# Kernel optimization log

Hardware: AMD Instinct MI355X
Metric: run time of the kernel (lower is better)

Reference implementation:

```python
import jax, jax.numpy as jnp
import numpy as np

N = 50000
E = 1600000
IN_DIM = 256
HID = 64
OUT = 16
NEG_SLOPE = 0.01


def setup_inputs() -> dict:
    key = jax.random.key(0)
    ks = jax.random.split(key, 6)
    local_features = jax.random.normal(ks[0], (N, IN_DIM), dtype=jnp.float32)
    edge_index = jax.random.randint(ks[1], (2, E), 0, N, dtype=jnp.int32)
    W0 = jax.random.normal(ks[2], (IN_DIM, HID), dtype=jnp.float32) * 0.05
    a0 = jax.random.normal(ks[3], (2 * HID, 1), dtype=jnp.float32) * 0.05
    W1 = jax.random.normal(ks[4], (HID, OUT), dtype=jnp.float32) * 0.05
    a1 = jax.random.normal(ks[5], (2 * OUT, 1), dtype=jnp.float32) * 0.05
    return {"local_features": local_features, "edge_index": edge_index,
            "W0": W0, "a0": a0, "W1": W1, "a1": a1}


def _segment_softmax(scores, seg, num_segments):
    # softmax over edges sharing the same row (destination) id
    smax = jax.ops.segment_max(scores, seg, num_segments=num_segments)
    ex = jnp.exp(scores - smax[seg])
    ssum = jax.ops.segment_sum(ex, seg, num_segments=num_segments)
    return ex / ssum[seg]


def _gat_layer(H, row, col, W, a, apply_elu):
    d = W.shape[1]
    Hw = H @ W                                   # [N, d]
    # score_e = leaky_relu([Hw[row] || Hw[col]] @ a) = leaky_relu(pr[row] + pc[col])
    pr = Hw @ a[:d, 0]                           # [N]
    pc = Hw @ a[d:, 0]                           # [N]
    s = pr[row] + pc[col]                        # [E]
    s = jnp.where(s >= 0, s, NEG_SLOPE * s)      # leaky_relu
    att = _segment_softmax(s, row, Hw.shape[0])  # per-row sparse softmax (dim=1)
    # out[row] = sum_e att_e * Hw[col_e]
    out = jax.ops.segment_sum(att[:, None] * Hw[col], row, num_segments=Hw.shape[0])
    if apply_elu:
        out = jnp.where(out > 0, out, jnp.expm1(out))  # elu
    return out


def reference(local_features, edge_index, W0, a0, W1, a1):
    row = edge_index[0]
    col = edge_index[1]
    H = _gat_layer(local_features, row, col, W0, a0, apply_elu=True)
    H = _gat_layer(H, row, col, W1, a1, apply_elu=False)
    return jax.nn.log_softmax(H, axis=1)
```

## Files before the change

### kernel.cpp

```cpp
#include <hip/hip_runtime.h>
#include <hip/hip_bf16.h>
#include <math.h>

#define NN 50000
#define NE 1600000
#define BSH 9
#define BCK 98
#define BCAP 20480

typedef __attribute__((ext_vector_type(8))) short bf16x8;
typedef __attribute__((ext_vector_type(4))) float f32x4;

__device__ __forceinline__ short f2bf(float f) {
    return (short)((__float_as_uint(f) + 0x8000u) >> 16);
}
__device__ __forceinline__ float bf2f(ushort u) {
    return __uint_as_float(((unsigned)u) << 16);
}
__device__ __forceinline__ unsigned enc_f(float f) {
    unsigned u = __float_as_uint(f);
    return (u & 0x80000000u) ? ~u : (u | 0x80000000u);
}
__device__ __forceinline__ float dec_f(unsigned e) {
    return (e & 0x80000000u) ? __uint_as_float(e & 0x7FFFFFFFu)
                             : __uint_as_float(~e);
}

__global__ void initcur_kernel(int* __restrict__ gcursor) {
    int b = threadIdx.x;
    if (b < BCK) gcursor[b] = b * BCAP;
}

__global__ void __launch_bounds__(1024) binA_kernel(
        const int* __restrict__ row, const int* __restrict__ col,
        int* __restrict__ gcursor, unsigned* __restrict__ staging) {
    __shared__ unsigned lds_stage[8192];
    __shared__ unsigned lds_addr[8192];
    __shared__ int lds_cnt[128];
    __shared__ int lds_off[128];
    __shared__ int wg_goff[128];
    __shared__ int wtot[2];
    int t = threadIdx.x;
    int lane = t & 63;
    int w = t >> 6;

    for (int cb = blockIdx.x * 8192; cb < NE; cb += gridDim.x * 8192) {
        int cnt_edges = NE - cb; if (cnt_edges > 8192) cnt_edges = 8192;
        if (t < 128) lds_cnt[t] = 0;
        __syncthreads();
        int myb[8]; int mylo[8]; unsigned mypk[8];
        #pragma unroll
        for (int i = 0; i < 8; ++i) {
            int idx = i * 1024 + t;
            myb[i] = -1;
            if (idx < cnt_edges) {
                int e = cb + idx;
                int r = row[e], c = col[e];
                int b = r >> BSH;
                myb[i] = b;
                mypk[i] = ((unsigned)(r & 511) << 16) | (unsigned)c;
                mylo[i] = atomicAdd(&lds_cnt[b], 1);
            }
        }
        __syncthreads();
        int v = (t < 128) ? lds_cnt[t] : 0;
        int x = v;
        #pragma unroll
        for (int off = 1; off < 64; off <<= 1) {
            int y = __shfl_up(x, off);
            if (lane >= off) x += y;
        }
        if (t < 128 && lane == 63) wtot[w] = x;
        __syncthreads();
        int add = (w == 1) ? wtot[0] : 0;
        if (t < 128) lds_off[t] = x - v + add;
        if (t < BCK) {
            int cc = lds_cnt[t];
            wg_goff[t] = cc ? atomicAdd(&gcursor[t], cc) : 0;
        }
        __syncthreads();
        #pragma unroll
        for (int i = 0; i < 8; ++i) if (myb[i] >= 0) {
            int p = lds_off[myb[i]] + mylo[i];
            lds_stage[p] = mypk[i];
            lds_addr[p] = (unsigned)(wg_goff[myb[i]] + mylo[i]);
        }
        __syncthreads();
        for (int i = t; i < cnt_edges; i += 1024)
            staging[lds_addr[i]] = lds_stage[i];
        __syncthreads();
    }
}

__global__ void bucketscan_kernel(const int* __restrict__ gcursor,
                                  int* __restrict__ bbase,
                                  int* __restrict__ rowptr) {
    __shared__ int wt0;
    int t = threadIdx.x;
    int lane = t & 63;
    int w = t >> 6;
    int v = (t < BCK) ? (gcursor[t] - t * BCAP) : 0;
    int x = v;
    #pragma unroll
    for (int off = 1; off < 64; off <<= 1) {
        int y = __shfl_up(x, off);
        if (lane >= off) x += y;
    }
    if (w == 0 && lane == 63) wt0 = x;
    __syncthreads();
    int excl = x - v + ((w == 1) ? wt0 : 0);
    if (t < BCK) bbase[t] = excl;
    if (t == BCK - 1) { bbase[BCK] = excl + v; rowptr[NN] = excl + v; }
}

__global__ void __launch_bounds__(1024) binB_kernel(
        const int* __restrict__ bbase,
        const unsigned* __restrict__ staging,
        int* __restrict__ rowptr,
        ushort* __restrict__ colperm) {
    __shared__ int cur[512];
    __shared__ int lexcl[512];
    __shared__ int wls[8];
    __shared__ ushort lds_col[BCAP];
    int b = blockIdx.x;
    int t = threadIdx.x;
    int lane = t & 63;
    int w = t >> 6;
    int rbase = b << BSH;
    int nrows = NN - rbase; if (nrows > 512) nrows = 512;
    int gbase = bbase[b];
    int cnt = bbase[b + 1] - gbase;
    if (cnt > BCAP) cnt = BCAP;
    const unsigned* sb = staging + (size_t)b * BCAP;

    if (t < 512) cur[t] = 0;
    __syncthreads();
    for (int i = t; i < cnt; i += 1024)
        atomicAdd(&cur[sb[i] >> 16], 1);
    __syncthreads();
    int v = 0, x = 0;
    if (t < 512) {
        v = cur[t];
        x = v;
        #pragma unroll
        for (int off = 1; off < 64; off <<= 1) {
            int y = __shfl_up(x, off);
            if (lane >= off) x += y;
        }
        if (lane == 63) wls[w] = x;
    }
    __syncthreads();
    if (t < 8) {
        int s = wls[t];
        #pragma unroll
        for (int off = 1; off < 8; off <<= 1) {
            int y = __shfl_up(s, off, 8);
            if ((t & 7) >= off) s += y;
        }
        wls[t] = s;
    }
    __syncthreads();
    if (t < 512) {
        int e = x - v + ((w > 0) ? wls[w - 1] : 0);
        lexcl[t] = e;
        if (t < nrows) rowptr[rbase + t] = gbase + e;
    }
    __syncthreads();
    if (t < 512) cur[t] = lexcl[t];
    __syncthreads();
    for (int i = t; i < cnt; i += 1024) {
        unsigned e = sb[i];
        int pos = atomicAdd(&cur[e >> 16], 1);
        lds_col[pos] = (ushort)(e & 0xFFFFu);
    }
    __syncthreads();
    for (int i = t; i < cnt; i += 1024)
        colperm[gbase + i] = lds_col[i];
}

__global__ void pcmax_kernel(const float* __restrict__ pc, unsigned* __restrict__ out) {
    int i = blockIdx.x * 256 + threadIdx.x;
    float v = (i < NN) ? pc[i] : -1e30f;
    #pragma unroll
    for (int off = 32; off; off >>= 1) v = fmaxf(v, __shfl_xor(v, off));
    if ((threadIdx.x & 63) == 0) atomicMax(out, enc_f(v));
}

__global__ void __launch_bounds__(256) gemm0_kernel(
        const float* __restrict__ X,
        const float* __restrict__ W,
        const float* __restrict__ a,
        __hip_bfloat16* __restrict__ Hwb,
        float* __restrict__ pr,
        float* __restrict__ pc) {
    __shared__ ushort Wt[64 * 264];
    int tid = threadIdx.x;
    int lane = tid & 63;
    int wid = tid >> 6;
    int c = lane & 15;
    int quad = lane >> 4;

    for (int i = tid; i < 256 * 64; i += 256) {
        int k = i >> 6, n = i & 63;
        Wt[n * 264 + k] = (ushort)f2bf(W[i]);
    }
    __syncthreads();

    int row0 = blockIdx.x * 64 + wid * 16;
    int arow = row0 + c; if (arow >= NN) arow = NN - 1;
    const float* xbase = X + (size_t)arow * 256 + quad * 8;
    const ushort* wt0 = &Wt[(0 * 16 + c) * 264 + quad * 8];
    const ushort* wt1 = &Wt[(1 * 16 + c) * 264 + quad * 8];
    const ushort* wt2 = &Wt[(2 * 16 + c) * 264 + quad * 8];
    const ushort* wt3 = &Wt[(3 * 16 + c) * 264 + quad * 8];

    f32x4 acc0 = {0.f,0.f,0.f,0.f}, acc1 = {0.f,0.f,0.f,0.f};
    f32x4 acc2 = {0.f,0.f,0.f,0.f}, acc3 = {0.f,0.f,0.f,0.f};

#pragma unroll
    for (int k0 = 0; k0 < 256; k0 += 32) {
        float4 xa = *(const float4*)(xbase + k0);
        float4 xb = *(const float4*)(xbase + k0 + 4);
        bf16x8 af;
        af[0] = f2bf(xa.x); af[1] = f2bf(xa.y); af[2] = f2bf(xa.z); af[3] = f2bf(xa.w);
        af[4] = f2bf(xb.x); af[5] = f2bf(xb.y); af[6] = f2bf(xb.z); af[7] = f2bf(xb.w);
        bf16x8 b0 = *(const bf16x8*)(wt0 + k0);
        bf16x8 b1 = *(const bf16x8*)(wt1 + k0);
        bf16x8 b2 = *(const bf16x8*)(wt2 + k0);
        bf16x8 b3 = *(const bf16x8*)(wt3 + k0);
        acc0 = __builtin_amdgcn_mfma_f32_16x16x32_bf16(af, b0, acc0, 0, 0, 0);
        acc1 = __builtin_amdgcn_mfma_f32_16x16x32_bf16(af, b1, acc1, 0, 0, 0);
        acc2 = __builtin_amdgcn_mfma_f32_16x16x32_bf16(af, b2, acc2, 0, 0, 0);
        acc3 = __builtin_amdgcn_mfma_f32_16x16x32_bf16(af, b3, acc3, 0, 0, 0);
    }

    float aA0 = a[c],      aA1 = a[16 + c],      aA2 = a[32 + c],      aA3 = a[48 + c];
    float aB0 = a[64 + c], aB1 = a[80 + c],      aB2 = a[96 + c],      aB3 = a[112 + c];

#pragma unroll
    for (int r = 0; r < 4; ++r) {
        int row = row0 + quad * 4 + r;
        float v0 = acc0[r], v1 = acc1[r], v2 = acc2[r], v3 = acc3[r];
        if (row < NN) {
            __hip_bfloat16* hp = Hwb + (size_t)row * 64 + c;
            hp[0]  = __float2bfloat16(v0);
            hp[16] = __float2bfloat16(v1);
            hp[32] = __float2bfloat16(v2);
            hp[48] = __float2bfloat16(v3);
        }
        float pv = v0 * aA0 + v1 * aA1 + v2 * aA2 + v3 * aA3;
        float qv = v0 * aB0 + v1 * aB1 + v2 * aB2 + v3 * aB3;
#pragma unroll
        for (int off = 8; off; off >>= 1) {
            pv += __shfl_xor(pv, off);
            qv += __shfl_xor(qv, off);
        }
        if (c == 0 && row < NN) { pr[row] = pv; pc[row] = qv; }
    }
}

__global__ void __launch_bounds__(256) node0_kernel(
        const int* __restrict__ rowptr,
        const ushort* __restrict__ colperm,
        const float* __restrict__ pr,
        const float* __restrict__ pc,
        const unsigned* __restrict__ pcmax,
        const ushort* __restrict__ Hwb,
        float* __restrict__ H1) {
    int lane = threadIdx.x & 63;
    int node = blockIdx.x * 4 + (threadIdx.x >> 6);
    if (node >= NN) return;
    int k = lane & 15, q = lane >> 4;
    int start = rowptr[node], end = rowptr[node + 1];
    float pri = pr[node];
    float m = pri + dec_f(*pcmax);
    m = (m >= 0.f) ? m : 0.01f * m;

    float wsum = 0.f;
    float acc0 = 0.f, acc1 = 0.f, acc2 = 0.f, acc3 = 0.f;
    for (int base = start; base < end; base += 64) {
        int n = end - base; if (n > 64) n = 64;
        float wv = 0.f; int cv = 0;
        if (lane < n) {
            cv = (int)colperm[base + lane];
            float s = pri + pc[cv];
            s = (s >= 0.f) ? s : 0.01f * s;
            wv = expf(s - m);
        }
        wsum += wv;
        int iters = (n + 3) >> 2;
        #pragma unroll 4
        for (int jj = 0; jj < iters; ++jj) {
            int j = jj * 4 + q;
            int jc = (j < n) ? j : 0;
            float wj = __shfl(wv, jc);
            if (j >= n) wj = 0.f;
            int cj = __shfl(cv, jc);
            ushort4 hv = *(const ushort4*)(Hwb + (size_t)cj * 64 + k * 4);
            acc0 = fmaf(wj, bf2f(hv.x), acc0);
            acc1 = fmaf(wj, bf2f(hv.y), acc1);
            acc2 = fmaf(wj, bf2f(hv.z), acc2);
            acc3 = fmaf(wj, bf2f(hv.w), acc3);
        }
    }
#pragma unroll
    for (int off = 32; off; off >>= 1) wsum += __shfl_xor(wsum, off);
    acc0 += __shfl_xor(acc0, 16); acc0 += __shfl_xor(acc0, 32);
    acc1 += __shfl_xor(acc1, 16); acc1 += __shfl_xor(acc1, 32);
    acc2 += __shfl_xor(acc2, 16); acc2 += __shfl_xor(acc2, 32);
    acc3 += __shfl_xor(acc3, 16); acc3 += __shfl_xor(acc3, 32);
    if (q == 0) {
        float inv = (wsum > 0.f) ? 1.f / wsum : 0.f;
        float4 o;
        float h;
        h = acc0 * inv; o.x = (h > 0.f) ? h : expm1f(h);
        h = acc1 * inv; o.y = (h > 0.f) ? h : expm1f(h);
        h = acc2 * inv; o.z = (h > 0.f) ? h : expm1f(h);
        h = acc3 * inv; o.w = (h > 0.f) ? h : expm1f(h);
        *(float4*)(H1 + (size_t)node * 64 + k * 4) = o;
    }
}

__global__ void gemm1_kernel(const float* __restrict__ H,
                             const float* __restrict__ W,
                             const float* __restrict__ a,
                             __hip_bfloat16* __restrict__ Hwb,
                             float* __restrict__ pr,
                             float* __restrict__ pc) {
    int tid = threadIdx.x;
    int j = tid & 15;
    int r = tid >> 4;
    int row = blockIdx.x * 16 + r;
    if (row >= NN) return;
    const float* h = H + (size_t)row * 64;
    float acc = 0.f;
#pragma unroll
    for (int k = 0; k < 64; ++k) acc += h[k] * W[k * 16 + j];
    Hwb[(size_t)row * 16 + j] = __float2bfloat16(acc);
    float prv = acc * a[j];
    float pcv = acc * a[16 + j];
    for (int off = 8; off; off >>= 1) {
        prv += __shfl_down(prv, off, 16);
        pcv += __shfl_down(pcv, off, 16);
    }
    if (j == 0) { pr[row] = prv; pc[row] = pcv; }
}

__global__ void __launch_bounds__(256) node1_kernel(
        const int* __restrict__ rowptr,
        const ushort* __restrict__ colperm,
        const float* __restrict__ pr,
        const float* __restrict__ pc,
        const unsigned* __restrict__ pcmax,
        const ushort* __restrict__ Hwb,
        float* __restrict__ out) {
    int lane = threadIdx.x & 63;
    int node = blockIdx.x * 4 + (threadIdx.x >> 6);
    if (node >= NN) return;
    int k = lane & 15, q = lane >> 4;
    int start = rowptr[node], end = rowptr[node + 1];
    float pri = pr[node];
    float m = pri + dec_f(*pcmax);
    m = (m >= 0.f) ? m : 0.01f * m;

    float wsum = 0.f, acc = 0.f;
    for (int base = start; base < end; base += 64) {
        int n = end - base; if (n > 64) n = 64;
        float wv = 0.f; int cv = 0;
        if (lane < n) {
            cv = (int)colperm[base + lane];
            float s = pri + pc[cv];
            s = (s >= 0.f) ? s : 0.01f * s;
            wv = expf(s - m);
        }
        wsum += wv;
        int iters = (n + 3) >> 2;
        #pragma unroll 4
        for (int jj = 0; jj < iters; ++jj) {
            int j = jj * 4 + q;
            int jc = (j < n) ? j : 0;
            float wj = __shfl(wv, jc);
            if (j >= n) wj = 0.f;
            int cj = __shfl(cv, jc);
            float hj = bf2f(Hwb[(size_t)cj * 16 + k]);
            acc = fmaf(wj, hj, acc);
        }
    }
#pragma unroll
    for (int off = 32; off; off >>= 1) wsum += __shfl_xor(wsum, off);
    acc += __shfl_xor(acc, 16);
    acc += __shfl_xor(acc, 32);
    float v = (wsum > 0.f) ? acc / wsum : 0.f;
    float mm = v;
#pragma unroll
    for (int off = 8; off; off >>= 1) mm = fmaxf(mm, __shfl_xor(mm, off, 16));
    float ex = expf(v - mm);
    float ssx = ex;
#pragma unroll
    for (int off = 8; off; off >>= 1) ssx += __shfl_xor(ssx, off, 16);
    float r = v - (mm + logf(ssx));
    if (lane < 16) out[(size_t)node * 16 + k] = r;
}

extern "C" void kernel_launch(void* const* d_in, const int* in_sizes, int n_in,
                              void* d_out, int out_size, void* d_ws, size_t ws_size,
                              hipStream_t stream) {
    const float* X  = (const float*)d_in[0];
    const int*   ei = (const int*)d_in[1];
    const float* W0 = (const float*)d_in[2];
    const float* a0 = (const float*)d_in[3];
    const float* W1 = (const float*)d_in[4];
    const float* a1 = (const float*)d_in[5];
    float* out = (float*)d_out;

    const int* row = ei;
    const int* col = ei + NE;

    char* wsb = (char*)d_ws;
    size_t off = 0;
    auto alloc = [&](size_t bytes) {
        void* p = wsb + off;
        off += (bytes + 15) & ~(size_t)15;
        return p;
    };
    unsigned* maxes = (unsigned*)alloc(16);
    int* rowptr     = (int*)alloc((NN + 2) * 4);
    int* gcursor    = (int*)alloc(128 * 4);
    int* bbase      = (int*)alloc(128 * 4);
    unsigned* staging = (unsigned*)alloc((size_t)BCK * BCAP * 4);
    ushort* colperm = (ushort*)alloc((size_t)NE * 2);
    __hip_bfloat16* Hw0b = (__hip_bfloat16*)alloc((size_t)NN * 64 * 2);
    float* pr0      = (float*)alloc(NN * 4);
    float* pc0      = (float*)alloc(NN * 4);
    float* H1       = (float*)alloc((size_t)NN * 64 * 4);
    __hip_bfloat16* Hw1b = (__hip_bfloat16*)alloc((size_t)NN * 16 * 2);
    float* pr1      = (float*)alloc(NN * 4);
    float* pc1      = (float*)alloc(NN * 4);

    hipMemsetAsync(maxes, 0, 16, stream);

    initcur_kernel<<<1, 128, 0, stream>>>(gcursor);
    binA_kernel<<<196, 1024, 0, stream>>>(row, col, gcursor, staging);
    bucketscan_kernel<<<1, 128, 0, stream>>>(gcursor, bbase, rowptr);
    binB_kernel<<<BCK, 1024, 0, stream>>>(bbase, staging, rowptr, colperm);

    gemm0_kernel<<<(NN + 63) / 64, 256, 0, stream>>>(X, W0, a0, Hw0b, pr0, pc0);
    pcmax_kernel<<<(NN + 255) / 256, 256, 0, stream>>>(pc0, &maxes[0]);
    node0_kernel<<<(NN + 3) / 4, 256, 0, stream>>>(rowptr, colperm, pr0, pc0,
                                                   &maxes[0], (const ushort*)Hw0b, H1);

    gemm1_kernel<<<(NN + 15) / 16, 256, 0, stream>>>(H1, W1, a1, Hw1b, pr1, pc1);
    pcmax_kernel<<<(NN + 255) / 256, 256, 0, stream>>>(pc1, &maxes[1]);
    node1_kernel<<<(NN + 3) / 4, 256, 0, stream>>>(rowptr, colperm, pr1, pc1,
                                                   &maxes[1], (const ushort*)Hw1b, out);
}
```

Measured before the change: 252.7 us.

## Fuse layer-1 projection into node0 epilogue and broadcast edge data via LDS

Computes H1 @ W1 and the layer-1 attention projections directly in the node0 epilogue using W1 cached in shared memory, removing the H1 intermediate buffer and the separate gemm1 launch. Both aggregation kernels now stage packed (weight, column) pairs in LDS instead of two cross-lane shuffles per edge iteration. This saves a large global round trip at the cost of extra LDS use and relies on intra-wavefront ordering without explicit barriers.

```diff
diff --git a/kernel.cpp b/kernel.cpp
--- a/kernel.cpp
+++ b/kernel.cpp
@@ -266,9 +266,24 @@
         const float* __restrict__ pc,
         const unsigned* __restrict__ pcmax,
         const ushort* __restrict__ Hwb,
-        float* __restrict__ H1) {
-    int lane = threadIdx.x & 63;
-    int node = blockIdx.x * 4 + (threadIdx.x >> 6);
+        const float* __restrict__ W1,
+        const float* __restrict__ a1,
+        __hip_bfloat16* __restrict__ Hw1b,
+        float* __restrict__ pr1,
+        float* __restrict__ pc1) {
+    __shared__ float W1s[64 * 17];
+    __shared__ float a1s[32];
+    __shared__ float hbuf[4][64];
+    __shared__ unsigned long long wcbuf[4][64];
+    int t = threadIdx.x;
+    for (int i = t; i < 64 * 16; i += 256)
+        W1s[(i >> 4) * 17 + (i & 15)] = W1[i];
+    if (t < 32) a1s[t] = a1[t];
+    __syncthreads();
+
+    int lane = t & 63;
+    int wid = t >> 6;
+    int node = blockIdx.x * 4 + wid;
     if (node >= NN) return;
     int k = lane & 15, q = lane >> 4;
     int start = rowptr[node], end = rowptr[node + 1];
@@ -280,22 +295,22 @@
     float acc0 = 0.f, acc1 = 0.f, acc2 = 0.f, acc3 = 0.f;
     for (int base = start; base < end; base += 64) {
         int n = end - base; if (n > 64) n = 64;
-        float wv = 0.f; int cv = 0;
+        float wv = 0.f; unsigned cv = 0;
         if (lane < n) {
-            cv = (int)colperm[base + lane];
+            cv = (unsigned)colperm[base + lane];
             float s = pri + pc[cv];
             s = (s >= 0.f) ? s : 0.01f * s;
             wv = expf(s - m);
         }
         wsum += wv;
+        wcbuf[wid][lane] = ((unsigned long long)cv << 32) |
+                           (unsigned long long)__float_as_uint(wv);
         int iters = (n + 3) >> 2;
         #pragma unroll 4
         for (int jj = 0; jj < iters; ++jj) {
-            int j = jj * 4 + q;
-            int jc = (j < n) ? j : 0;
-            float wj = __shfl(wv, jc);
-            if (j >= n) wj = 0.f;
-            int cj = __shfl(cv, jc);
+            unsigned long long wc = wcbuf[wid][jj * 4 + q];
+            float wj = __uint_as_float((unsigned)wc);
+            int cj = (int)(wc >> 32);
             ushort4 hv = *(const ushort4*)(Hwb + (size_t)cj * 64 + k * 4);
             acc0 = fmaf(wj, bf2f(hv.x), acc0);
             acc1 = fmaf(wj, bf2f(hv.y), acc1);
@@ -309,41 +324,34 @@
     acc1 += __shfl_xor(acc1, 16); acc1 += __shfl_xor(acc1, 32);
     acc2 += __shfl_xor(acc2, 16); acc2 += __shfl_xor(acc2, 32);
     acc3 += __shfl_xor(acc3, 16); acc3 += __shfl_xor(acc3, 32);
+
+    float inv = (wsum > 0.f) ? 1.f / wsum : 0.f;
+    float h0 = acc0 * inv; h0 = (h0 > 0.f) ? h0 : expm1f(h0);
+    float h1 = acc1 * inv; h1 = (h1 > 0.f) ? h1 : expm1f(h1);
+    float h2 = acc2 * inv; h2 = (h2 > 0.f) ? h2 : expm1f(h2);
+    float h3 = acc3 * inv; h3 = (h3 > 0.f) ? h3 : expm1f(h3);
     if (q == 0) {
-        float inv = (wsum > 0.f) ? 1.f / wsum : 0.f;
-        float4 o;
-        float h;
-        h = acc0 * inv; o.x = (h > 0.f) ? h : expm1f(h);
-        h = acc1 * inv; o.y = (h > 0.f) ? h : expm1f(h);
-        h = acc2 * inv; o.z = (h > 0.f) ? h : expm1f(h);
-        h = acc3 * inv; o.w = (h > 0.f) ? h : expm1f(h);
-        *(float4*)(H1 + (size_t)node * 64 + k * 4) = o;
-    }
-}
-
-__global__ void gemm1_kernel(const float* __restrict__ H,
-                             const float* __restrict__ W,
-                             const float* __restrict__ a,
-                             __hip_bfloat16* __restrict__ Hwb,
-                             float* __restrict__ pr,
-                             float* __restrict__ pc) {
-    int tid = threadIdx.x;
-    int j = tid & 15;
-    int r = tid >> 4;
-    int row = blockIdx.x * 16 + r;
-    if (row >= NN) return;
-    const float* h = H + (size_t)row * 64;
-    float acc = 0.f;
-#pragma unroll
-    for (int k = 0; k < 64; ++k) acc += h[k] * W[k * 16 + j];
-    Hwb[(size_t)row * 16 + j] = __float2bfloat16(acc);
-    float prv = acc * a[j];
-    float pcv = acc * a[16 + j];
+        float4 hh = {h0, h1, h2, h3};
+        *(float4*)&hbuf[wid][k * 4] = hh;
+    }
+    float vj = 0.f;
+    const float* hb = hbuf[wid];
+#pragma unroll
+    for (int i = 0; i < 16; ++i) {
+        int kk = q * 16 + i;
+        vj = fmaf(hb[kk], W1s[kk * 17 + k], vj);
+    }
+    vj += __shfl_xor(vj, 16);
+    vj += __shfl_xor(vj, 32);
+    if (q == 0) Hw1b[(size_t)node * 16 + k] = __float2bfloat16(vj);
+    float pv = vj * a1s[k];
+    float qv = vj * a1s[16 + k];
+#pragma unroll
     for (int off = 8; off; off >>= 1) {
-        prv += __shfl_down(prv, off, 16);
-        pcv += __shfl_down(pcv, off, 16);
-    }
-    if (j == 0) { pr[row] = prv; pc[row] = pcv; }
+        pv += __shfl_xor(pv, off);
+        qv += __shfl_xor(qv, off);
+    }
+    if (lane == 0) { pr1[node] = pv; pc1[node] = qv; }
 }
 
 __global__ void __launch_bounds__(256) node1_kernel(
@@ -354,8 +362,10 @@
         const unsigned* __restrict__ pcmax,
         const ushort* __restrict__ Hwb,
         float* __restrict__ out) {
+    __shared__ unsigned long long wcbuf[4][64];
     int lane = threadIdx.x & 63;
-    int node = blockIdx.x * 4 + (threadIdx.x >> 6);
+    int wid = threadIdx.x >> 6;
+    int node = blockIdx.x * 4 + wid;
     if (node >= NN) return;
     int k = lane & 15, q = lane >> 4;
     int start = rowptr[node], end = rowptr[node + 1];
@@ -366,22 +376,22 @@
     float wsum = 0.f, acc = 0.f;
     for (int base = start; base < end; base += 64) {
         int n = end - base; if (n > 64) n = 64;
-        float wv = 0.f; int cv = 0;
+        float wv = 0.f; unsigned cv = 0;
         if (lane < n) {
-            cv = (int)colperm[base + lane];
+            cv = (unsigned)colperm[base + lane];
             float s = pri + pc[cv];
             s = (s >= 0.f) ? s : 0.01f * s;
             wv = expf(s - m);
         }
         wsum += wv;
+        wcbuf[wid][lane] = ((unsigned long long)cv << 32) |
+                           (unsigned long long)__float_as_uint(wv);
         int iters = (n + 3) >> 2;
         #pragma unroll 4
         for (int jj = 0; jj < iters; ++jj) {
-            int j = jj * 4 + q;
-            int jc = (j < n) ? j : 0;
-            float wj = __shfl(wv, jc);
-            if (j >= n) wj = 0.f;
-            int cj = __shfl(cv, jc);
+            unsigned long long wc = wcbuf[wid][jj * 4 + q];
+            float wj = __uint_as_float((unsigned)wc);
+            int cj = (int)(wc >> 32);
             float hj = bf2f(Hwb[(size_t)cj * 16 + k]);
             acc = fmaf(wj, hj, acc);
         }
@@ -432,7 +442,6 @@
     __hip_bfloat16* Hw0b = (__hip_bfloat16*)alloc((size_t)NN * 64 * 2);
     float* pr0      = (float*)alloc(NN * 4);
     float* pc0      = (float*)alloc(NN * 4);
-    float* H1       = (float*)alloc((size_t)NN * 64 * 4);
     __hip_bfloat16* Hw1b = (__hip_bfloat16*)alloc((size_t)NN * 16 * 2);
     float* pr1      = (float*)alloc(NN * 4);
     float* pc1      = (float*)alloc(NN * 4);
@@ -447,9 +456,9 @@
     gemm0_kernel<<<(NN + 63) / 64, 256, 0, stream>>>(X, W0, a0, Hw0b, pr0, pc0);
     pcmax_kernel<<<(NN + 255) / 256, 256, 0, stream>>>(pc0, &maxes[0]);
     node0_kernel<<<(NN + 3) / 4, 256, 0, stream>>>(rowptr, colperm, pr0, pc0,
-                                                   &maxes[0], (const ushort*)Hw0b, H1);
-
-    gemm1_kernel<<<(NN + 15) / 16, 256, 0, stream>>>(H1, W1, a1, Hw1b, pr1, pc1);
+                                                   &maxes[0], (const ushort*)Hw0b,
+                                                   W1, a1, Hw1b, pr1, pc1);
+
     pcmax_kernel<<<(NN + 255) / 256, 256, 0, stream>>>(pc1, &maxes[1]);
     node1_kernel<<<(NN + 3) / 4, 256, 0, stream>>>(rowptr, colperm, pr1, pc1,
                                                    &maxes[1], (const ushort*)Hw1b, out);
```

Result: faster. 229.6 us (-9.2%).
